# Performance work log

Measured on AMD Instinct MI355X. Metric: run time of the kernel, lower is better.

The kernel has to match this reference:

```python
import jax, jax.numpy as jnp
import numpy as np
from jax import lax

SEQ_LEN = 8192
N_FEATURES = 1
E = 128            # embedding_dim
H1 = 2 * E         # 256
H2 = 4 * E         # 512


def _lstm_params(key, in_dim, hidden):
    k1, k2, k3, k4 = jax.random.split(key, 4)
    s = 1.0 / np.sqrt(hidden)
    return (
        jax.random.uniform(k1, (4 * hidden, in_dim), jnp.float32, -s, s),   # Wih
        jax.random.uniform(k2, (4 * hidden, hidden), jnp.float32, -s, s),   # Whh
        jax.random.uniform(k3, (4 * hidden,), jnp.float32, -s, s),          # bih
        jax.random.uniform(k4, (4 * hidden,), jnp.float32, -s, s),          # bhh
    )


def lstm(x, Wih, Whh, bih, bhh):
    """Single-layer PyTorch-convention LSTM over x:[T,in]. Returns (ys:[T,H], h_T:[H])."""
    H = Whh.shape[1]
    # precompute input contribution for all timesteps (memory-bound GEMM once)
    xg = x @ Wih.T + (bih + bhh)  # [T, 4H]

    def step(carry, gx):
        h, c = carry
        g = gx + h @ Whh.T
        i, f, gc, o = jnp.split(g, 4)
        i = jax.nn.sigmoid(i)
        f = jax.nn.sigmoid(f)
        gc = jnp.tanh(gc)
        o = jax.nn.sigmoid(o)
        c = f * c + i * gc
        h = o * jnp.tanh(c)
        return (h, c), h

    init = (jnp.zeros((H,), x.dtype), jnp.zeros((H,), x.dtype))
    (hT, _), ys = lax.scan(step, init, xg)
    return ys, hT


def setup_inputs() -> dict:
    key = jax.random.key(0)
    keys = jax.random.split(key, 8)
    inp = {"x": jax.random.normal(keys[0], (SEQ_LEN, N_FEATURES), jnp.float32)}
    # encoder: n_features -> H2 -> H1 -> E
    for name, k, din, dh in [("e1", keys[1], N_FEATURES, H2), ("e2", keys[2], H2, H1), ("e3", keys[3], H1, E),
                             ("d1", keys[4], E, E), ("d2", keys[5], E, H1), ("d3", keys[6], H1, H2)]:
        Wih, Whh, bih, bhh = _lstm_params(k, din, dh)
        inp[name + "_Wih"], inp[name + "_Whh"], inp[name + "_bih"], inp[name + "_bhh"] = Wih, Whh, bih, bhh
    ko1, ko2 = jax.random.split(keys[7])
    s = 1.0 / np.sqrt(H2)
    inp["out_W"] = jax.random.uniform(ko1, (N_FEATURES, H2), jnp.float32, -s, s)
    inp["out_b"] = jax.random.uniform(ko2, (N_FEATURES,), jnp.float32, -s, s)
    return inp


def reference(x,
              e1_Wih, e1_Whh, e1_bih, e1_bhh,
              e2_Wih, e2_Whh, e2_bih, e2_bhh,
              e3_Wih, e3_Whh, e3_bih, e3_bhh,
              d1_Wih, d1_Whh, d1_bih, d1_bhh,
              d2_Wih, d2_Whh, d2_bih, d2_bhh,
              d3_Wih, d3_Whh, d3_bih, d3_bhh,
              out_W, out_b):
    # --- encoder ---
    xs = x.reshape(SEQ_LEN, N_FEATURES)
    ys, _ = lstm(xs, e1_Wih, e1_Whh, e1_bih, e1_bhh)   # [T, H2]
    ys, _ = lstm(ys, e2_Wih, e2_Whh, e2_bih, e2_bhh)   # [T, H1]
    _, hT = lstm(ys, e3_Wih, e3_Whh, e3_bih, e3_bhh)   # hT: [E]
    z = hT.reshape(N_FEATURES, E)                       # [1, E]
    # --- decoder: repeat latent across time ---
    zr = jnp.tile(z.reshape(1, E), (SEQ_LEN, 1))        # [T, E]
    ys, _ = lstm(zr, d1_Wih, d1_Whh, d1_bih, d1_bhh)    # [T, E]
    ys, _ = lstm(ys, d2_Wih, d2_Whh, d2_bih, d2_bhh)    # [T, H1]
    ys, _ = lstm(ys, d3_Wih, d3_Whh, d3_bih, d3_bhh)    # [T, H2]
    return ys @ out_W.T + out_b                          # [T, 1]
```

## Files before the change

kernel.cpp:

```cpp
#include <hip/hip_runtime.h>
#include <stdint.h>

#define T_LEN 8192

__device__ __forceinline__ float sigf(float x) {
    return 1.0f / (1.0f + __expf(-x));
}
__device__ __forceinline__ float tanh_fast(float x) {
    float e = __expf(2.0f * x);
    return 1.0f - 2.0f / (e + 1.0f);
}

template<int H, int NWG, int TPB, int SUBS, int XGMODE, int LID, bool WRITE_YS, bool WRITE_Z>
__global__ __launch_bounds__(TPB)
void lstm_scan(const float* __restrict__ Whh,
               const float* __restrict__ xg,
               const float* __restrict__ wih0,
               const float* __restrict__ bih,
               const float* __restrict__ bhh,
               float* __restrict__ ys,
               unsigned long long* __restrict__ hst,
               float* __restrict__ zout)
{
    constexpr int ROWS = 4 * H / NWG;
    constexpr int HJ   = H / NWG;
    constexpr int CH   = H / SUBS;
    constexpr int CHP  = CH + 8;
    static_assert(ROWS * SUBS == TPB, "bad layout");

    const int tid = threadIdx.x;
    const int wg  = (NWG > 1) ? blockIdx.x : 0;
    const int q   = tid / SUBS;
    const int sub = tid % SUBS;
    const int g   = q / HJ;
    const int jj  = q % HJ;
    const int grow = g * H + wg * HJ + jj;

    __shared__ float hbuf[SUBS * CHP];
    __shared__ float act[ROWS];
    __shared__ int abortf;

    float4 wreg[CH / 4];
    {
        const float4* wr = (const float4*)(Whh + (size_t)grow * H + sub * CH);
        #pragma unroll
        for (int i = 0; i < CH / 4; ++i) wreg[i] = wr[i];
    }

    float w0 = 0.f, bs = 0.f, xg_const = 0.f;
    if constexpr (XGMODE == 1) { w0 = wih0[grow]; bs = bih[grow] + bhh[grow]; }
    if constexpr (XGMODE == 2) { xg_const = xg[grow]; }

    float c = 0.f;
    for (int k = tid; k < SUBS * CHP; k += TPB) hbuf[k] = 0.f;
    if (tid == 0) abortf = 0;
    __syncthreads();

    for (int t = 0; t < T_LEN; ++t) {
        float xgv = 0.f;
        if (sub == 0) {
            if constexpr (XGMODE == 0)      xgv = xg[(size_t)t * (4 * H) + grow];
            else if constexpr (XGMODE == 1) xgv = fmaf(xg[t], w0, bs);
            else                            xgv = xg_const;
        }
        if constexpr (NWG > 1) {
            if (t > 0 && tid < H) {
                const size_t idx = (size_t)(t - 1) * H + tid;
                const unsigned want = (unsigned)(LID * T_LEN + t);
                unsigned long long v;
                int spin = 0;
                for (;;) {
                    v = __hip_atomic_load(&hst[idx], __ATOMIC_RELAXED,
                                          __HIP_MEMORY_SCOPE_AGENT);
                    if ((unsigned)(v >> 32) == want) break;
                    if (++spin >= (1 << 20)) { abortf = 1; break; }
                }
                union { unsigned u; float f; } cv;
                cv.u = (unsigned)v;
                hbuf[(tid / CH) * CHP + (tid % CH)] = cv.f;
            }
        }
        __syncthreads();
        if (abortf) break;

        float4 a4 = make_float4(0.f, 0.f, 0.f, 0.f);
        const float4* hv4 = (const float4*)&hbuf[sub * CHP];
        #pragma unroll
        for (int i = 0; i < CH / 4; ++i) {
            float4 hv = hv4[i];
            float4 wv = wreg[i];
            a4.x = fmaf(wv.x, hv.x, a4.x);
            a4.y = fmaf(wv.y, hv.y, a4.y);
            a4.z = fmaf(wv.z, hv.z, a4.z);
            a4.w = fmaf(wv.w, hv.w, a4.w);
        }
        float acc = (a4.x + a4.y) + (a4.z + a4.w);
        #pragma unroll
        for (int d = 1; d < SUBS; d <<= 1) acc += __shfl_xor(acc, d);

        if (sub == 0) {
            float gv = acc + xgv;
            act[q] = (g == 2) ? tanh_fast(gv) : sigf(gv);
        }
        __syncthreads();

        if (tid < HJ) {
            float iv = act[tid];
            float fv = act[HJ + tid];
            float gc = act[2 * HJ + tid];
            float ov = act[3 * HJ + tid];
            c = fmaf(fv, c, iv * gc);
            float h = ov * tanh_fast(c);
            if constexpr (WRITE_YS) ys[(size_t)t * H + wg * HJ + tid] = h;
            if constexpr (NWG > 1) {
                union { float f; unsigned u; } cv;
                cv.f = h;
                unsigned long long pk =
                    ((unsigned long long)(unsigned)(LID * T_LEN + t + 1) << 32) | cv.u;
                __hip_atomic_store(&hst[(size_t)t * H + wg * HJ + tid], pk,
                                   __ATOMIC_RELAXED, __HIP_MEMORY_SCOPE_AGENT);
            } else {
                hbuf[(tid / CH) * CHP + (tid % CH)] = h;
            }
            if constexpr (WRITE_Z) { if (t == T_LEN - 1) zout[tid] = h; }
        }
        __syncthreads();
    }
}

__global__ __launch_bounds__(256)
void gemm_bias(const float* __restrict__ A, const float* __restrict__ B,
               const float* __restrict__ bih, const float* __restrict__ bhh,
               float* __restrict__ C, int M, int N, int K)
{
    __shared__ float As[16][72];
    __shared__ float Bs[16][72];
    const int tid = threadIdx.x;
    const int bm = blockIdx.y * 64;
    const int bn = blockIdx.x * 64;
    const int tm = (tid / 16) * 4;
    const int tn = (tid % 16) * 4;
    const int lr = tid >> 2;
    const int lc = (tid & 3) * 4;
    float acc[4][4] = {{0.f}};
    for (int k0 = 0; k0 < K; k0 += 16) {
        float4 va = *(const float4*)&A[(size_t)(bm + lr) * K + k0 + lc];
        float4 vb = *(const float4*)&B[(size_t)(bn + lr) * K + k0 + lc];
        As[lc + 0][lr] = va.x; As[lc + 1][lr] = va.y;
        As[lc + 2][lr] = va.z; As[lc + 3][lr] = va.w;
        Bs[lc + 0][lr] = vb.x; Bs[lc + 1][lr] = vb.y;
        Bs[lc + 2][lr] = vb.z; Bs[lc + 3][lr] = vb.w;
        __syncthreads();
        #pragma unroll
        for (int kk = 0; kk < 16; ++kk) {
            float4 av = *(const float4*)&As[kk][tm];
            float4 bv = *(const float4*)&Bs[kk][tn];
            float ar[4] = {av.x, av.y, av.z, av.w};
            float br[4] = {bv.x, bv.y, bv.z, bv.w};
            #pragma unroll
            for (int i = 0; i < 4; ++i)
                #pragma unroll
                for (int j = 0; j < 4; ++j)
                    acc[i][j] = fmaf(ar[i], br[j], acc[i][j]);
        }
        __syncthreads();
    }
    float bsum[4];
    #pragma unroll
    for (int j = 0; j < 4; ++j) bsum[j] = bih[bn + tn + j] + bhh[bn + tn + j];
    #pragma unroll
    for (int i = 0; i < 4; ++i) {
        float4 o;
        o.x = acc[i][0] + bsum[0];
        o.y = acc[i][1] + bsum[1];
        o.z = acc[i][2] + bsum[2];
        o.w = acc[i][3] + bsum[3];
        *(float4*)&C[(size_t)(bm + tm + i) * N + bn + tn] = o;
    }
}

__global__ __launch_bounds__(512)
void xg_const_d1(const float* __restrict__ z, const float* __restrict__ Wih,
                 const float* __restrict__ bih, const float* __restrict__ bhh,
                 float* __restrict__ xgd1)
{
    __shared__ float zs[128];
    const int tid = threadIdx.x;
    if (tid < 128) zs[tid] = z[tid];
    __syncthreads();
    const float4* wr = (const float4*)(Wih + (size_t)tid * 128);
    float4 a4 = make_float4(0.f, 0.f, 0.f, 0.f);
    #pragma unroll
    for (int i = 0; i < 32; ++i) {
        float4 w = wr[i];
        float4 h = *(const float4*)&zs[i * 4];
        a4.x = fmaf(w.x, h.x, a4.x); a4.y = fmaf(w.y, h.y, a4.y);
        a4.z = fmaf(w.z, h.z, a4.z); a4.w = fmaf(w.w, h.w, a4.w);
    }
    xgd1[tid] = (a4.x + a4.y) + (a4.z + a4.w) + bih[tid] + bhh[tid];
}

__global__ __launch_bounds__(256)
void out_gemv(const float* __restrict__ ys, const float* __restrict__ Wo,
              const float* __restrict__ bo, float* __restrict__ out)
{
    const int lane = threadIdx.x & 63;
    const int wid  = threadIdx.x >> 6;
    const int t = blockIdx.x * 4 + wid;
    const float* row = ys + (size_t)t * 512;
    float a = 0.f;
    #pragma unroll
    for (int i = 0; i < 8; ++i) a = fmaf(row[lane + i * 64], Wo[lane + i * 64], a);
    #pragma unroll
    for (int d = 1; d < 64; d <<= 1) a += __shfl_xor(a, d);
    if (lane == 0) out[t] = a + bo[0];
}

template<int H, int NWG, int TPB, int SUBS, int XGMODE, int LID, bool YS, bool Z>
static void launch_scan(const float* whh, const float* xg, const float* wih0,
                        const float* bih, const float* bhh, float* ys,
                        unsigned long long* hst, float* zout, hipStream_t stream)
{
    auto kfn = lstm_scan<H, NWG, TPB, SUBS, XGMODE, LID, YS, Z>;
    if (NWG > 1) {
        void* args[8] = {&whh, &xg, &wih0, &bih, &bhh, &ys, &hst, &zout};
        hipError_t e = hipLaunchCooperativeKernel(reinterpret_cast<void*>(kfn),
                                                  dim3(NWG), dim3(TPB), args, 0u, stream);
        if (e == hipSuccess) return;
    }
    kfn<<<dim3(NWG), dim3(TPB), 0, stream>>>(whh, xg, wih0, bih, bhh, ys, hst, zout);
}

extern "C" void kernel_launch(void* const* d_in, const int* in_sizes, int n_in,
                              void* d_out, int out_size, void* d_ws, size_t ws_size,
                              hipStream_t stream)
{
    (void)in_sizes; (void)n_in; (void)out_size;
    const float* x = (const float*)d_in[0];
    const float* Wih[6]; const float* Whh[6]; const float* Bih[6]; const float* Bhh[6];
    for (int l = 0; l < 6; ++l) {
        Wih[l] = (const float*)d_in[1 + l * 4 + 0];
        Whh[l] = (const float*)d_in[1 + l * 4 + 1];
        Bih[l] = (const float*)d_in[1 + l * 4 + 2];
        Bhh[l] = (const float*)d_in[1 + l * 4 + 3];
    }
    const float* outW = (const float*)d_in[25];
    const float* outb = (const float*)d_in[26];

    char* ws = (char*)d_ws;
    float* XG  = (float*)(ws);
    float* ysA = (float*)(ws + ((size_t)64 << 20));
    float* ysB = (float*)(ws + ((size_t)80 << 20));
    unsigned long long* HST = (unsigned long long*)(ws + ((size_t)96 << 20));
    float* z    = (float*)(ws + ((size_t)128 << 20));
    float* xgd1 = (float*)(ws + ((size_t)128 << 20) + 1024);
    if (ws_size < (((size_t)128 << 20) + 4096)) return;

    launch_scan<512, 32, 512, 8, 1, 1, true, false>(Whh[0], x, Wih[0], Bih[0], Bhh[0],
                                                    ysA, HST, nullptr, stream);
    gemm_bias<<<dim3(1024 / 64, T_LEN / 64), 256, 0, stream>>>(ysA, Wih[1], Bih[1], Bhh[1],
                                                               XG, T_LEN, 1024, 512);
    launch_scan<256, 16, 512, 8, 0, 2, true, false>(Whh[1], XG, nullptr, nullptr, nullptr,
                                                    ysB, HST, nullptr, stream);
    gemm_bias<<<dim3(512 / 64, T_LEN / 64), 256, 0, stream>>>(ysB, Wih[2], Bih[2], Bhh[2],
                                                              XG, T_LEN, 512, 256);
    launch_scan<128, 1, 512, 1, 0, 0, false, true>(Whh[2], XG, nullptr, nullptr, nullptr,
                                                   nullptr, nullptr, z, stream);

    xg_const_d1<<<1, 512, 0, stream>>>(z, Wih[3], Bih[3], Bhh[3], xgd1);
    launch_scan<128, 1, 512, 1, 2, 0, true, false>(Whh[3], xgd1, nullptr, nullptr, nullptr,
                                                   ysA, nullptr, nullptr, stream);
    gemm_bias<<<dim3(1024 / 64, T_LEN / 64), 256, 0, stream>>>(ysA, Wih[4], Bih[4], Bhh[4],
                                                               XG, T_LEN, 1024, 128);
    launch_scan<256, 16, 512, 8, 0, 3, true, false>(Whh[4], XG, nullptr, nullptr, nullptr,
                                                    ysB, HST, nullptr, stream);
    gemm_bias<<<dim3(2048 / 64, T_LEN / 64), 256, 0, stream>>>(ysB, Wih[5], Bih[5], Bhh[5],
                                                               XG, T_LEN, 2048, 256);
    launch_scan<512, 32, 512, 8, 0, 4, true, false>(Whh[5], XG, nullptr, nullptr, nullptr,
                                                    ysA, HST, nullptr, stream);

    out_gemv<<<dim3(T_LEN / 4), 256, 0, stream>>>(ysA, outW, outb, (float*)d_out);
}
```

Baseline: 64.57 ms.

## Interleave gate rows per wave and double-buffer hidden state to drop a barrier

Thread-to-row mapping changes so the four gates of each hidden unit sit in the same wave. The cell update then gathers i/f/g/o with shuffles instead of going through shared memory plus an extra __syncthreads. The hidden-state buffer is double-buffered so each step needs only one barrier, and each workgroup writes its own h locally instead of spinning on global memory for it. The change also prefetches the next step's xg, stages the scalar input sequence in LDS, and adds a min-blocks launch bound. The costs are more shared memory and a new reliance on wave-level layout assumptions.

After: 71.00 ms. 10.0% more time.

```diff
diff --git a/kernel.cpp b/kernel.cpp
--- a/kernel.cpp
+++ b/kernel.cpp
@@ -12,7 +12,7 @@
 }
 
 template<int H, int NWG, int TPB, int SUBS, int XGMODE, int LID, bool WRITE_YS, bool WRITE_Z>
-__global__ __launch_bounds__(TPB)
+__global__ __launch_bounds__(TPB, TPB / 256)
 void lstm_scan(const float* __restrict__ Whh,
                const float* __restrict__ xg,
                const float* __restrict__ wih0,
@@ -25,19 +25,20 @@
     constexpr int ROWS = 4 * H / NWG;
     constexpr int HJ   = H / NWG;
     constexpr int CH   = H / SUBS;
-    constexpr int CHP  = CH + 8;
+    constexpr int CHP  = CH + 4;
     static_assert(ROWS * SUBS == TPB, "bad layout");
+    static_assert(4 * SUBS <= 64, "gate group must fit a wave");
 
     const int tid = threadIdx.x;
     const int wg  = (NWG > 1) ? blockIdx.x : 0;
     const int q   = tid / SUBS;
     const int sub = tid % SUBS;
-    const int g   = q / HJ;
-    const int jj  = q % HJ;
+    const int jj  = q >> 2;
+    const int g   = q & 3;
     const int grow = g * H + wg * HJ + jj;
 
-    __shared__ float hbuf[SUBS * CHP];
-    __shared__ float act[ROWS];
+    __shared__ float hbuf[2 * SUBS * CHP];
+    __shared__ float xsh[XGMODE == 1 ? T_LEN : 1];
     __shared__ int abortf;
 
     float4 wreg[CH / 4];
@@ -47,24 +48,31 @@
         for (int i = 0; i < CH / 4; ++i) wreg[i] = wr[i];
     }
 
-    float w0 = 0.f, bs = 0.f, xg_const = 0.f;
+    float w0 = 0.f, bs = 0.f, xgc = 0.f;
     if constexpr (XGMODE == 1) { w0 = wih0[grow]; bs = bih[grow] + bhh[grow]; }
-    if constexpr (XGMODE == 2) { xg_const = xg[grow]; }
-
+    if constexpr (XGMODE == 2) { xgc = xg[grow]; }
+    if constexpr (XGMODE == 1) {
+        for (int k = tid; k < T_LEN; k += TPB) xsh[k] = xg[k];
+    }
+
+    for (int k = tid; k < 2 * SUBS * CHP; k += TPB) hbuf[k] = 0.f;
+    if (tid == 0) abortf = 0;
+
+    const bool writer = (tid % (4 * SUBS)) == 0;
+    const int  wjj    = tid / (4 * SUBS);
     float c = 0.f;
-    for (int k = tid; k < SUBS * CHP; k += TPB) hbuf[k] = 0.f;
-    if (tid == 0) abortf = 0;
-    __syncthreads();
+
+    float xgv = 0.f;
+    if constexpr (XGMODE == 0) { if (sub == 0) xgv = xg[grow]; }
 
     for (int t = 0; t < T_LEN; ++t) {
-        float xgv = 0.f;
-        if (sub == 0) {
-            if constexpr (XGMODE == 0)      xgv = xg[(size_t)t * (4 * H) + grow];
-            else if constexpr (XGMODE == 1) xgv = fmaf(xg[t], w0, bs);
-            else                            xgv = xg_const;
-        }
+        float xgn = 0.f;
+        if constexpr (XGMODE == 0) {
+            if (sub == 0 && t + 1 < T_LEN) xgn = xg[(size_t)(t + 1) * (4 * H) + grow];
+        }
+
         if constexpr (NWG > 1) {
-            if (t > 0 && tid < H) {
+            if (t > 0 && tid < H && (tid / HJ) != wg) {
                 const size_t idx = (size_t)(t - 1) * H + tid;
                 const unsigned want = (unsigned)(LID * T_LEN + t);
                 unsigned long long v;
@@ -73,21 +81,21 @@
                     v = __hip_atomic_load(&hst[idx], __ATOMIC_RELAXED,
                                           __HIP_MEMORY_SCOPE_AGENT);
                     if ((unsigned)(v >> 32) == want) break;
-                    if (++spin >= (1 << 20)) { abortf = 1; break; }
+                    if (++spin >= (1 << 22)) { abortf = 1; break; }
                 }
                 union { unsigned u; float f; } cv;
                 cv.u = (unsigned)v;
-                hbuf[(tid / CH) * CHP + (tid % CH)] = cv.f;
+                hbuf[(t & 1) * SUBS * CHP + (tid / CH) * CHP + (tid % CH)] = cv.f;
             }
         }
         __syncthreads();
-        if (abortf) break;
-
+        if constexpr (NWG > 1) { if (abortf) break; }
+
+        const float* hb = &hbuf[(t & 1) * SUBS * CHP + sub * CHP];
         float4 a4 = make_float4(0.f, 0.f, 0.f, 0.f);
-        const float4* hv4 = (const float4*)&hbuf[sub * CHP];
         #pragma unroll
         for (int i = 0; i < CH / 4; ++i) {
-            float4 hv = hv4[i];
+            float4 hv = *(const float4*)&hb[i * 4];
             float4 wv = wreg[i];
             a4.x = fmaf(wv.x, hv.x, a4.x);
             a4.y = fmaf(wv.y, hv.y, a4.y);
@@ -98,33 +106,34 @@
         #pragma unroll
         for (int d = 1; d < SUBS; d <<= 1) acc += __shfl_xor(acc, d);
 
-        if (sub == 0) {
-            float gv = acc + xgv;
-            act[q] = (g == 2) ? tanh_fast(gv) : sigf(gv);
-        }
-        __syncthreads();
-
-        if (tid < HJ) {
-            float iv = act[tid];
-            float fv = act[HJ + tid];
-            float gc = act[2 * HJ + tid];
-            float ov = act[3 * HJ + tid];
-            c = fmaf(fv, c, iv * gc);
+        float base;
+        if constexpr (XGMODE == 0)      base = xgv;
+        else if constexpr (XGMODE == 1) base = fmaf(xsh[t], w0, bs);
+        else                            base = xgc;
+        float gv = acc + base;
+        float av = (g == 2) ? tanh_fast(gv) : sigf(gv);
+
+        float fv = __shfl_down(av, SUBS);
+        float gc = __shfl_down(av, 2 * SUBS);
+        float ov = __shfl_down(av, 3 * SUBS);
+
+        if (writer) {
+            c = fmaf(fv, c, av * gc);
             float h = ov * tanh_fast(c);
-            if constexpr (WRITE_YS) ys[(size_t)t * H + wg * HJ + tid] = h;
+            const int e = wg * HJ + wjj;
+            hbuf[((t + 1) & 1) * SUBS * CHP + (e / CH) * CHP + (e % CH)] = h;
+            if constexpr (WRITE_YS) ys[(size_t)t * H + e] = h;
             if constexpr (NWG > 1) {
                 union { float f; unsigned u; } cv;
                 cv.f = h;
                 unsigned long long pk =
                     ((unsigned long long)(unsigned)(LID * T_LEN + t + 1) << 32) | cv.u;
-                __hip_atomic_store(&hst[(size_t)t * H + wg * HJ + tid], pk,
+                __hip_atomic_store(&hst[(size_t)t * H + e], pk,
                                    __ATOMIC_RELAXED, __HIP_MEMORY_SCOPE_AGENT);
-            } else {
-                hbuf[(tid / CH) * CHP + (tid % CH)] = h;
             }
-            if constexpr (WRITE_Z) { if (t == T_LEN - 1) zout[tid] = h; }
-        }
-        __syncthreads();
+            if constexpr (WRITE_Z) { if (t == T_LEN - 1) zout[e] = h; }
+        }
+        if constexpr (XGMODE == 0) xgv = xgn;
     }
 }
 
```
